# Kernel optimization log

Measured on AMD Instinct MI355X. Metric: run time of the kernel, lower is better.

## Reference

```python
import jax, jax.numpy as jnp
import numpy as np

B = 1024        # interactions per batch (graphs per side)
DIM = 64        # args.dim
HID = 64        # args.hidd_dim == args.word_dim
L = 2           # args.num_layers
NREL = 4        # relation types
N_USERS, N_ITEMS, N_WORDS = 100000, 50000, 50000
N = 131072      # total nodes per batched graph (per side)
E = 524288      # total edges per batched graph (per side)
D_FM = (L + 1) * DIM * 2  # 384


def setup_inputs() -> dict:
    key = jax.random.key(0)
    ks = iter(jax.random.split(key, 64))
    nrm = lambda shape, s=0.05: jax.random.normal(next(ks), shape, jnp.float32) * s
    ri = lambda shape, hi: jax.random.randint(next(ks), shape, 0, hi)
    # deterministic sorted graph-membership vector: equal-size graphs, no empty segments
    batch = (jnp.arange(N) * B) // N
    return dict(
        uid=ri((B,), N_USERS), iid=ri((B,), N_ITEMS),
        u_nodes=ri((N,), N_WORDS), i_nodes=ri((N,), N_WORDS),
        u_edge_index=ri((2, E), N), i_edge_index=ri((2, E), N),
        u_edge_type=ri((E,), NREL), i_edge_type=ri((E,), NREL),
        u_batch=batch, i_batch=batch,
        user_emb=nrm((N_USERS, DIM)), item_emb=nrm((N_ITEMS, DIM)), word_emb=nrm((N_WORDS, HID)),
        trans_u_W=nrm((L, DIM, HID)), trans_u_b=jnp.zeros((L, HID)),
        trans_i_W=nrm((L, DIM, HID)), trans_i_b=jnp.zeros((L, HID)),
        trans_w_W=nrm((L, HID, DIM)), trans_w_b=jnp.zeros((L, DIM)),
        inter_u_W=nrm((DIM, DIM)), inter_u_b=jnp.zeros((DIM,)),
        inter_i_W=nrm((DIM, DIM)), inter_i_b=jnp.zeros((DIM,)),
        conv_u_W=nrm((L, HID, HID)), conv_u_b=jnp.zeros((L, HID)),
        conv_u_att=nrm((L, 3, HID)), conv_u_rel=nrm((L, NREL, HID)),
        conv_i_W=nrm((L, HID, HID)), conv_i_b=jnp.zeros((L, HID)),
        conv_i_att=nrm((L, 3, HID)), conv_i_rel=nrm((L, NREL, HID)),
        pool_W=nrm((HID, HID)),
        fm_w=nrm((D_FM,)), fm_V=nrm((D_FM, D_FM)),
        fm_bias_u=jnp.zeros((N_USERS,)), fm_bias_i=jnp.zeros((N_ITEMS,)), fm_bias=jnp.zeros((1,)),
    )


def _gat(x, ei, et, W, b, att, rel):
    """Relational GAT conv: attention over incoming edges with relation-type term."""
    n = x.shape[0]
    h = x @ W + b                         # [n, HID]
    src, dst = ei[0], ei[1]
    e = jax.nn.leaky_relu(h[src] @ att[0] + h[dst] @ att[1] + rel[et] @ att[2], 0.2)  # [E]
    emax = jax.ops.segment_max(e, dst, num_segments=n)
    emax = jnp.where(jnp.isfinite(emax), emax, 0.0)   # guard nodes with no in-edges
    ex = jnp.exp(e - emax[dst])
    den = jax.ops.segment_sum(ex, dst, num_segments=n)
    alpha = ex / (den[dst] + 1e-16)
    return jax.nn.relu(jax.ops.segment_sum(alpha[:, None] * h[src], dst, num_segments=n))


def _conv_pool(ui_em, x, ei, et, batch, Ws, bs, atts, rels, tw_W, tw_b, pool_W, nb):
    """L stages of GAT conv -> query-conditioned soft pooling gate -> global max pool."""
    inv_sqrt_d = 1.0 / np.sqrt(HID).astype(np.float32)
    outs = []
    for i in range(L):
        x = _gat(x, ei, et, Ws[i], bs[i], atts[i], rels[i])
        q = ui_em[i]                                          # [B, HID] per-graph query
        score = jax.nn.sigmoid(jnp.sum((x @ pool_W) * q[batch], -1) * inv_sqrt_d)  # [N]
        x = x * score[:, None]
        pooled = jax.ops.segment_max(x, batch, num_segments=nb)  # gmp -> [B, HID]
        outs.append(jax.nn.relu(pooled @ tw_W[i] + tw_b[i]))     # trans_w -> [B, DIM]
    return jnp.concatenate(outs, -1)                             # [B, L*DIM]


def reference(uid, iid, u_nodes, i_nodes, u_edge_index, i_edge_index,
              u_edge_type, i_edge_type, u_batch, i_batch,
              user_emb, item_emb, word_emb,
              trans_u_W, trans_u_b, trans_i_W, trans_i_b, trans_w_W, trans_w_b,
              inter_u_W, inter_u_b, inter_i_W, inter_i_b,
              conv_u_W, conv_u_b, conv_u_att, conv_u_rel,
              conv_i_W, conv_i_b, conv_i_att, conv_i_rel,
              pool_W, fm_w, fm_V, fm_bias_u, fm_bias_i, fm_bias):
    u_e = user_emb[uid]                                        # [B, DIM]
    i_e = item_emb[iid]
    u_em = [jax.nn.relu(u_e @ trans_u_W[i] + trans_u_b[i]) for i in range(L)]
    i_em = [jax.nn.relu(i_e @ trans_i_W[i] + trans_i_b[i]) for i in range(L)]
    u_pool = _conv_pool(u_em, word_emb[u_nodes], u_edge_index, u_edge_type, u_batch,
                        conv_u_W, conv_u_b, conv_u_att, conv_u_rel,
                        trans_w_W, trans_w_b, pool_W, B)
    i_pool = _conv_pool(i_em, word_emb[i_nodes], i_edge_index, i_edge_type, i_batch,
                        conv_i_W, conv_i_b, conv_i_att, conv_i_rel,
                        trans_w_W, trans_w_b, pool_W, B)
    user_rep = jax.nn.relu(u_e @ inter_u_W + inter_u_b)
    item_rep = jax.nn.relu(i_e @ inter_i_W + inter_i_b)
    x = jnp.concatenate([user_rep, u_pool, item_rep, i_pool], -1)   # [B, D_FM]
    # FM layer (degree-2 interaction with full V matrix, as in source)
    linear = x @ fm_w                                               # [B]
    xv = x @ fm_V                                                   # [B, D_FM]
    mlp = 0.5 * jnp.sum(xv * xv - (x * x) @ (fm_V * fm_V), -1)
    return linear + mlp + fm_bias_u[uid] + fm_bias_i[iid] + fm_bias[0]
```

## Files before the change

kernel.cpp:

```cpp
#include <hip/hip_runtime.h>
#include <hip/hip_bf16.h>

#define NN 131072
#define NE 524288
#define NB 1024

typedef __attribute__((ext_vector_type(8))) short short8;
typedef __attribute__((ext_vector_type(4))) float f32x4;

__device__ __forceinline__ float wsum(float v){
#pragma unroll
  for (int o = 32; o > 0; o >>= 1) v += __shfl_xor(v, o, 64);
  return v;
}
__device__ __forceinline__ short f2bs(float f){
  __hip_bfloat16 t = __float2bfloat16(f);
  union { __hip_bfloat16 b; short s; } u; u.b = t; return u.s;
}
__device__ __forceinline__ float bs2f(short s){
  return __uint_as_float(((unsigned)(unsigned short)s) << 16);
}
__device__ __forceinline__ float ulo2f(unsigned v){ return __uint_as_float(v << 16); }
__device__ __forceinline__ float uhi2f(unsigned v){ return __uint_as_float(v & 0xFFFF0000u); }
__device__ __forceinline__ unsigned fpack(float x, float y){
  return (unsigned)(unsigned short)f2bs(x) | ((unsigned)(unsigned short)f2bs(y) << 16);
}

__global__ void k_mega(int wconvB,
                       const int* __restrict__ u_ei, const int* __restrict__ i_ei,
                       int* __restrict__ cnt, int* __restrict__ loff,
                       const float* __restrict__ wemb, unsigned* __restrict__ wtab,
                       int n32,
                       const float* __restrict__ cuW, const float* __restrict__ ciW,
                       const float* __restrict__ pW,
                       const float* __restrict__ cub, const float* __restrict__ cib,
                       const float* __restrict__ uatt, const float* __restrict__ iatt,
                       const float* __restrict__ urel, const float* __restrict__ irel,
                       short8* __restrict__ frag, float* __restrict__ waA,
                       float* __restrict__ ba, float* __restrict__ rtab,
                       const int* __restrict__ uid, const int* __restrict__ iid,
                       const float* __restrict__ uemb, const float* __restrict__ iemb,
                       const float* __restrict__ uiW, const float* __restrict__ uib,
                       const float* __restrict__ iiW, const float* __restrict__ iib,
                       const float* __restrict__ utW, const float* __restrict__ utb,
                       const float* __restrict__ itW, const float* __restrict__ itb,
                       float* __restrict__ xfm, float* __restrict__ q){
  const int histB = 2 * NE / 256;
  int blk = blockIdx.x, tid = threadIdx.x;
  if (blk < histB){
    int ee = blk * 256 + tid;
    int side = ee >= NE;
    int e = ee - side * NE;
    const int* ei = side ? i_ei : u_ei;
    int dst = ei[NE + e] + side * NN;
    int p = atomicAdd(&cnt[dst], 1);
    loff[ee] = p;
  } else if (blk < histB + 10){
    int b2 = blk - histB;
    int mat = b2 >> 1;
    const float* W = mat < 2 ? cuW + mat * 4096 : (mat < 4 ? ciW + (mat - 2) * 4096 : pW);
    int g = (b2 & 1) * 256 + tid;
    int lane = g & 63, rest = g >> 6;
    int hh = rest & 1, t = rest >> 1;
    int m = lane & 15, qq = lane >> 4;
    short8 v;
#pragma unroll
    for (int j = 0; j < 8; j++)
      v[j] = f2bs(W[(hh * 32 + qq * 8 + j) * 64 + (t * 16 + m)]);
    frag[mat * 512 + g] = v;
  } else if (blk < histB + 12){
    int side = blk - histB - 10;
    const float* W    = side ? ciW : cuW;
    const float* bias = side ? cib : cub;
    const float* att  = side ? iatt : uatt;
    const float* rel  = side ? irel : urel;
    int l = tid >> 7, a = (tid >> 6) & 1, kk = tid & 63;
    float s = 0.f;
    for (int c = 0; c < 64; c++) s += W[l * 4096 + kk * 64 + c] * att[l * 192 + a * 64 + c];
    waA[((side * 2 + l) * 2 + a) * 64 + kk] = s;
    if (tid < 4){
      int l2 = tid >> 1, a2 = tid & 1;
      float sb = 0.f;
      for (int c = 0; c < 64; c++) sb += bias[l2 * 64 + c] * att[l2 * 192 + a2 * 64 + c];
      ba[(side * 2 + l2) * 2 + a2] = sb;
    }
    if (tid >= 4 && tid < 12){
      int id = tid - 4, l2 = id >> 2, tt = id & 3;
      float sr = 0.f;
      for (int c = 0; c < 64; c++) sr += rel[l2 * 256 + tt * 64 + c] * att[l2 * 192 + 128 + c];
      rtab[(side * 2 + l2) * 4 + tt] = sr;
    }
  } else if (blk < histB + 12 + wconvB){
    int id = (blk - histB - 12) * 256 + tid;
    if (id < n32){
      const float2* src = (const float2*)wemb;
      float2 v = src[id];
      wtab[id] = fpack(v.x, v.y);
    }
  } else {
    int lane = tid & 63, w = tid >> 6;
    int b = (blk - histB - 12 - wconvB) * 4 + w;
    int side = b >= NB;
    int lb = b - side * NB;
    const int* ids = side ? iid : uid;
    const float* emb = side ? iemb : uemb;
    const float* interW = side ? iiW : uiW;
    const float* interB = side ? iib : uib;
    const float* transW = side ? itW : utW;
    const float* transB = side ? itb : utb;
    int repOff = side ? 192 : 0;
    float xe = emb[(long)ids[lb] * 64 + lane];
    float o = interB[lane];
#pragma unroll
    for (int k = 0; k < 64; k++) o += __shfl(xe, k, 64) * interW[k * 64 + lane];
    xfm[lb * 384 + repOff + lane] = fmaxf(o, 0.f);
    for (int l = 0; l < 2; l++){
      float t = transB[l * 64 + lane];
#pragma unroll
      for (int k = 0; k < 64; k++) t += __shfl(xe, k, 64) * transW[l * 4096 + k * 64 + lane];
      q[((size_t)(side * 2 + l) * NB + lb) * 64 + lane] = fmaxf(t, 0.f);
    }
  }
}

__global__ void k_scan1(const int* __restrict__ cnt, int* __restrict__ rowptr,
                        int* __restrict__ bsum){
  __shared__ int sh[256];
  int i = blockIdx.x * 256 + threadIdx.x;
  int v = cnt[i];
  sh[threadIdx.x] = v; __syncthreads();
  for (int off = 1; off < 256; off <<= 1){
    int t = (threadIdx.x >= off) ? sh[threadIdx.x - off] : 0;
    __syncthreads();
    sh[threadIdx.x] += t;
    __syncthreads();
  }
  int incl = sh[threadIdx.x];
  rowptr[i] = incl - v;
  if (threadIdx.x == 255) bsum[blockIdx.x] = incl;
}

__global__ void k_scan2(int* __restrict__ bsum){
  __shared__ int sh[1024];
  int v = bsum[threadIdx.x];
  sh[threadIdx.x] = v; __syncthreads();
  for (int off = 1; off < 1024; off <<= 1){
    int t = (threadIdx.x >= off) ? sh[threadIdx.x - off] : 0;
    __syncthreads();
    sh[threadIdx.x] += t;
    __syncthreads();
  }
  bsum[threadIdx.x] = sh[threadIdx.x] - v;
}

__global__ void k_scan3(int* __restrict__ rowptr, const int* __restrict__ bsum){
  int i = blockIdx.x * 256 + threadIdx.x;
  int v = rowptr[i] + bsum[blockIdx.x];
  rowptr[i] = v;
  if (i == 0) rowptr[2 * NN] = 2 * NE;
}

__global__ void k_scw(const int* __restrict__ u_ei, const int* __restrict__ i_ei,
                      const int* __restrict__ u_et, const int* __restrict__ i_et,
                      const int* __restrict__ rowptr, const int* __restrict__ loff,
                      int* __restrict__ pedge,
                      const short* __restrict__ wtab, int nwords,
                      const float* __restrict__ waA, const float* __restrict__ ba,
                      float* __restrict__ wa0, float* __restrict__ wa1){
  const int scatB = 2 * NE / 256;
  int blk = blockIdx.x, tid = threadIdx.x;
  if (blk < scatB){
    int ee = blk * 256 + tid;
    int side = ee >= NE;
    int e = ee - side * NE;
    const int* ei = side ? i_ei : u_ei;
    const int* et = side ? i_et : u_et;
    int dst = ei[NE + e] + side * NN;
    int src = ei[e] + side * NN;
    int p = rowptr[dst] + loff[ee];
    pedge[p] = src | (et[e] << 18);
  } else {
    int lane = tid & 63, w = tid >> 6;
    int q = lane >> 4, cl = lane & 15;
    int sw0 = ((blk - scatB) * 4 + w) * 8;
    const uint2* wt2 = (const uint2*)wtab;
    for (int it = 0; it < 2; it++){
      int wj = sw0 + it * 4 + q;
      if (wj >= 2 * nwords) continue;
      int side = wj >= nwords;
      int wid = wj - side * nwords;
      const float* A0 = waA + (side * 2 + 0) * 2 * 64;
      const float* A1 = A0 + 64;
      uint2 v = wt2[(long)wid * 16 + cl];
      int d = 4 * cl;
      float p0 = ulo2f(v.x) * A0[d] + uhi2f(v.x) * A0[d + 1] +
                 ulo2f(v.y) * A0[d + 2] + uhi2f(v.y) * A0[d + 3];
      float p1 = ulo2f(v.x) * A1[d] + uhi2f(v.x) * A1[d + 1] +
                 ulo2f(v.y) * A1[d + 2] + uhi2f(v.y) * A1[d + 3];
      p0 += __shfl_xor(p0, 1, 64); p0 += __shfl_xor(p0, 2, 64);
      p0 += __shfl_xor(p0, 4, 64); p0 += __shfl_xor(p0, 8, 64);
      p1 += __shfl_xor(p1, 1, 64); p1 += __shfl_xor(p1, 2, 64);
      p1 += __shfl_xor(p1, 4, 64); p1 += __shfl_xor(p1, 8, 64);
      if (cl == 0){
        wa0[(size_t)side * nwords + wid] = p0 + ba[side * 4 + 0];
        wa1[(size_t)side * nwords + wid] = p1 + ba[side * 4 + 1];
      }
    }
  }
}

template<int L>
__device__ __forceinline__ void dev_agg(
    const int* __restrict__ rowptr, const int* __restrict__ pedge,
    const float* __restrict__ a0, const float* __restrict__ a1,
    const float* __restrict__ wa0, const float* __restrict__ wa1,
    const int* __restrict__ u_nodes, const int* __restrict__ i_nodes, int nwords,
    const float* __restrict__ rtab, const short* __restrict__ rows,
    unsigned* __restrict__ xo32){
  int lane = threadIdx.x & 63, w = threadIdx.x >> 6;
  int nb = (blockIdx.x * 4 + w) * 8;
  int side = nb >= NN;
  const float* rt = rtab + (side * 2 + L) * 4;
  float rt0 = rt[0], rt1 = rt[1], rt2 = rt[2], rt3 = rt[3];
  const int* nodesS = side ? i_nodes : u_nodes;
  const float* wa0S = wa0 + (size_t)side * nwords;
  const float* wa1S = wa1 + (size_t)side * nwords;
  int q = lane >> 4, cl = lane & 15;
  int rp = (lane < 9) ? rowptr[nb + lane] : 0;
  float a1v = 0.f;
  if (L == 0){
    if (lane < 8) a1v = wa1S[nodesS[nb + lane - side * NN]];
  } else {
    if (lane < 8) a1v = a1[nb + lane];
  }
  int rp0 = __shfl(rp, 0, 64);
  int rp8 = __shfl(rp, 8, 64);
  int tot = min(rp8 - rp0, 64);
  int eidx = rp0 + lane;
  int pe = (lane < tot) ? pedge[eidx] : 0;
  int psrc = pe & 0x3FFFF;
  int prow; float pa0 = 0.f;
  if (L == 0){
    int wid = (lane < tot) ? nodesS[psrc - side * NN] : 0;
    prow = wid;
    if (lane < tot) pa0 = wa0S[wid];
  } else {
    prow = psrc;
    if (lane < tot) pa0 = a0[psrc];
  }
  int kn = 0;
#pragma unroll
  for (int t = 1; t < 8; t++)
    kn += (eidx >= __shfl(rp, t, 64)) ? 1 : 0;
  float a1n = __shfl(a1v, kn, 64);
  int pet = (pe >> 18) & 3;
  float rr = (pet & 2) ? ((pet & 1) ? rt3 : rt2) : ((pet & 1) ? rt1 : rt0);
  float vv = pa0 + a1n + rr;
  vv = (vv > 0.f) ? vv : 0.2f * vv;
  float pex = (lane < tot) ? __expf(vv) : 0.f;
  const uint2* h2 = (const uint2*)rows;
#pragma unroll
  for (int k = 0; k < 8; k++){
    int r0 = __shfl(rp, k, 64), r1 = __shfl(rp, k + 1, 64);
    float a1k = __shfl(a1v, k, 64);
    float ax0 = 0.f, ay0 = 0.f, ax1 = 0.f, ay1 = 0.f, den = 0.f;
    for (int j = r0; j < r1; j += 4){
      int e = j + q;
      bool ok = e < r1;
      int idx = e - rp0;
      int idxc = min(idx, 63);
      int s = __shfl(prow, idxc, 64);
      float ex = __shfl(pex, idxc, 64);
      if (idx >= 64 && ok){
        int pe2 = pedge[e];
        int s2 = pe2 & 0x3FFFF;
        int et2 = (pe2 >> 18) & 3;
        float r2 = (et2 & 2) ? ((et2 & 1) ? rt3 : rt2) : ((et2 & 1) ? rt1 : rt0);
        float av;
        if (L == 0){ int wid = nodesS[s2 - side * NN]; av = wa0S[wid]; s = wid; }
        else       { av = a0[s2]; s = s2; }
        float v2 = av + a1k + r2;
        v2 = (v2 > 0.f) ? v2 : 0.2f * v2;
        ex = __expf(v2);
      }
      if (ok){
        uint2 v = h2[(long)s * 16 + cl];
        ax0 += ex * ulo2f(v.x); ay0 += ex * uhi2f(v.x);
        ax1 += ex * ulo2f(v.y); ay1 += ex * uhi2f(v.y);
        den += ex;
      }
    }
    ax0 += __shfl_xor(ax0, 16, 64); ax0 += __shfl_xor(ax0, 32, 64);
    ay0 += __shfl_xor(ay0, 16, 64); ay0 += __shfl_xor(ay0, 32, 64);
    ax1 += __shfl_xor(ax1, 16, 64); ax1 += __shfl_xor(ax1, 32, 64);
    ay1 += __shfl_xor(ay1, 16, 64); ay1 += __shfl_xor(ay1, 32, 64);
    den += __shfl_xor(den, 16, 64); den += __shfl_xor(den, 32, 64);
    float inv = 1.f / (den + 1e-16f);
    if (q == 0){
      uint2 o;
      o.x = fpack(ax0 * inv, ay0 * inv);
      o.y = fpack(ax1 * inv, ay1 * inv);
      ((uint2*)xo32)[(long)(nb + k) * 16 + cl] = o;
    }
  }
}

__global__ __launch_bounds__(256) void k_agg0(
    const int* __restrict__ rowptr, const int* __restrict__ pedge,
    const float* __restrict__ wa0, const float* __restrict__ wa1,
    const int* __restrict__ u_nodes, const int* __restrict__ i_nodes, int nwords,
    const float* __restrict__ rtab, const short* __restrict__ wtab,
    unsigned* __restrict__ xo32){
  dev_agg<0>(rowptr, pedge, nullptr, nullptr, wa0, wa1, u_nodes, i_nodes, nwords,
             rtab, wtab, xo32);
}

__global__ __launch_bounds__(256) void k_agg1(
    const int* __restrict__ rowptr, const int* __restrict__ pedge,
    const float* __restrict__ a0, const float* __restrict__ a1,
    const float* __restrict__ rtab, const short* __restrict__ x,
    unsigned* __restrict__ xo32){
  dev_agg<1>(rowptr, pedge, a0, a1, nullptr, nullptr, nullptr, nullptr, 0,
             rtab, x, xo32);
}

__global__ __launch_bounds__(256) void k_gp(
    int l, const short* __restrict__ xagg, const short8* __restrict__ frag,
    const float* __restrict__ cub, const float* __restrict__ cib,
    const float* __restrict__ waA_all, const float* __restrict__ ba_all,
    const float* __restrict__ qbuf, const float* __restrict__ twW_all,
    const float* __restrict__ twb_all, float* __restrict__ xfm,
    short* __restrict__ xnext, float* __restrict__ a0, float* __restrict__ a1){
  __shared__ short xt[128 * 72];
  __shared__ float gates[128];
  __shared__ float red[4][64];
  int b = blockIdx.x;
  int side = b >= NB;
  int g = b - side * NB;
  long base = (long)side * NN + (long)g * 128;
  int tid = threadIdx.x, lane = tid & 63, w = tid >> 6;
  int m = lane & 15, q = lane >> 4;
  const short8* wfrag = frag + (side * 2 + l) * 512;
  const float* bias = (side ? cib : cub) + l * 64;
  short8 Bf[4][2];
#pragma unroll
  for (int t = 0; t < 4; t++)
#pragma unroll
    for (int hh = 0; hh < 2; hh++)
      Bf[t][hh] = wfrag[(t * 2 + hh) * 64 + lane];
  float bs[4];
#pragma unroll
  for (int t = 0; t < 4; t++) bs[t] = bias[t * 16 + m];
  f32x4 accA[2][4];
#pragma unroll
  for (int rb = 0; rb < 2; rb++){
    long n0 = base + w * 32 + rb * 16;
    const short8* xr = (const short8*)(xagg + (n0 + m) * 64);
    short8 A0 = xr[q];
    short8 A1 = xr[q + 4];
#pragma unroll
    for (int t = 0; t < 4; t++){
      f32x4 acc = (f32x4){bs[t], bs[t], bs[t], bs[t]};
      acc = __builtin_amdgcn_mfma_f32_16x16x32_bf16(A0, Bf[t][0], acc, 0, 0, 0);
      acc = __builtin_amdgcn_mfma_f32_16x16x32_bf16(A1, Bf[t][1], acc, 0, 0, 0);
#pragma unroll
      for (int r = 0; r < 4; r++) acc[r] = fmaxf(acc[r], 0.f);
      accA[rb][t] = acc;
#pragma unroll
      for (int r = 0; r < 4; r++)
        xt[(w * 32 + rb * 16 + q * 4 + r) * 72 + t * 16 + m] = f2bs(acc[r]);
    }
  }
  __syncthreads();
  const short8* pfrag = frag + 4 * 512;
  const float* qv_ = qbuf + ((size_t)(side * 2 + l) * NB + g) * 64;
  short8 Pf[4][2];
#pragma unroll
  for (int t = 0; t < 4; t++)
#pragma unroll
    for (int hh = 0; hh < 2; hh++)
      Pf[t][hh] = pfrag[(t * 2 + hh) * 64 + lane];
  float qv[4];
#pragma unroll
  for (int t = 0; t < 4; t++) qv[t] = qv_[t * 16 + m];
#pragma unroll
  for (int rb = 0; rb < 2; rb++){
    int rowb = w * 32 + rb * 16;
    short8 A0 = *(const short8*)(xt + (rowb + m) * 72 + q * 8);
    short8 A1 = *(const short8*)(xt + (rowb + m) * 72 + 32 + q * 8);
    f32x4 accp[4];
#pragma unroll
    for (int t = 0; t < 4; t++){
      accp[t] = (f32x4){0.f, 0.f, 0.f, 0.f};
      accp[t] = __builtin_amdgcn_mfma_f32_16x16x32_bf16(A0, Pf[t][0], accp[t], 0, 0, 0);
      accp[t] = __builtin_amdgcn_mfma_f32_16x16x32_bf16(A1, Pf[t][1], accp[t], 0, 0, 0);
    }
#pragma unroll
    for (int r = 0; r < 4; r++){
      float p = accp[0][r] * qv[0] + accp[1][r] * qv[1] +
                accp[2][r] * qv[2] + accp[3][r] * qv[3];
      p += __shfl_xor(p, 1, 64); p += __shfl_xor(p, 2, 64);
      p += __shfl_xor(p, 4, 64); p += __shfl_xor(p, 8, 64);
      if (m == 0)
        gates[rowb + q * 4 + r] = 1.f / (1.f + __expf(-p * 0.125f));
    }
  }
  __syncthreads();
  const unsigned* xt32 = (const unsigned*)xt;
  int c = lane & 31, half = lane >> 5;
  float mxx = 0.f, mxy = 0.f;
#pragma unroll
  for (int p = 0; p < 16; p++){
    int nn = w * 32 + 2 * p + half;
    unsigned v = xt32[nn * 36 + c];
    float gt = gates[nn];
    mxx = fmaxf(mxx, ulo2f(v) * gt);
    mxy = fmaxf(mxy, uhi2f(v) * gt);
  }
  mxx = fmaxf(mxx, __shfl_xor(mxx, 32, 64));
  mxy = fmaxf(mxy, __shfl_xor(mxy, 32, 64));
  if (half == 0){ red[w][2 * c] = mxx; red[w][2 * c + 1] = mxy; }
  __syncthreads();
  if (tid < 64){
    const float* twW = twW_all + l * 4096;
    const float* twb = twb_all + l * 64;
    int off = (side ? 256 : 64) + l * 64;
    float p = fmaxf(fmaxf(red[0][tid], red[1][tid]), fmaxf(red[2][tid], red[3][tid]));
    float o = twb[tid];
    red[0][tid] = p;
    __syncwarp();
    for (int d = 0; d < 64; d++) o += red[0][d] * twW[d * 64 + tid];
    xfm[g * 384 + off + tid] = fmaxf(o, 0.f);
  }
  if (l == 0){
#pragma unroll
    for (int p = 0; p < 4; p++){
      int row = p * 32 + (tid >> 3);
      int col8 = (tid & 7) * 8;
      float gt = gates[row];
      short8 v = *(const short8*)(xt + row * 72 + col8);
      short8 o;
#pragma unroll
      for (int j = 0; j < 8; j++) o[j] = f2bs(bs2f(v[j]) * gt);
      *(short8*)(xnext + (base + row) * 64 + col8) = o;
    }
    const float* wn0p = waA_all + ((side * 2 + 1) * 2 + 0) * 64;
    const float* wn1p = wn0p + 64;
    float wn0[4], wn1[4];
#pragma unroll
    for (int t = 0; t < 4; t++){ wn0[t] = wn0p[t * 16 + m]; wn1[t] = wn1p[t * 16 + m]; }
    float ban0 = ba_all[(side * 2 + 1) * 2 + 0];
    float ban1 = ba_all[(side * 2 + 1) * 2 + 1];
#pragma unroll
    for (int rb = 0; rb < 2; rb++)
#pragma unroll
      for (int r = 0; r < 4; r++){
        float p0 = accA[rb][0][r] * wn0[0] + accA[rb][1][r] * wn0[1] +
                   accA[rb][2][r] * wn0[2] + accA[rb][3][r] * wn0[3];
        float p1 = accA[rb][0][r] * wn1[0] + accA[rb][1][r] * wn1[1] +
                   accA[rb][2][r] * wn1[2] + accA[rb][3][r] * wn1[3];
        p0 += __shfl_xor(p0, 1, 64); p0 += __shfl_xor(p0, 2, 64);
        p0 += __shfl_xor(p0, 4, 64); p0 += __shfl_xor(p0, 8, 64);
        p1 += __shfl_xor(p1, 1, 64); p1 += __shfl_xor(p1, 2, 64);
        p1 += __shfl_xor(p1, 4, 64); p1 += __shfl_xor(p1, 8, 64);
        if (m == 0){
          int row = w * 32 + rb * 16 + q * 4 + r;
          float gr = gates[row];
          a0[base + row] = p0 * gr + ban0;
          a1[base + row] = p1 * gr + ban1;
        }
      }
  }
}

__global__ __launch_bounds__(384) void k_fm(
    const float* __restrict__ xfm, const float* __restrict__ V,
    const float* __restrict__ fw, const float* __restrict__ bu,
    const float* __restrict__ bi, const float* __restrict__ b0,
    const int* __restrict__ uid, const int* __restrict__ iid,
    float* __restrict__ out){
  __shared__ float xsh[4][384];
  __shared__ float xsq[4][384];
  __shared__ float part[4][384];
  int j = threadIdx.x;
  int g0 = blockIdx.x * 4;
#pragma unroll
  for (int b = 0; b < 4; b++){
    float xv_ = xfm[(g0 + b) * 384 + j];
    xsh[b][j] = xv_;
    xsq[b][j] = xv_ * xv_;
  }
  __syncthreads();
  float xv[4] = {0.f, 0.f, 0.f, 0.f};
  float vv[4] = {0.f, 0.f, 0.f, 0.f};
  for (int k = 0; k < 384; k++){
    float v = V[(size_t)k * 384 + j];
    float v2 = v * v;
#pragma unroll
    for (int b = 0; b < 4; b++){
      xv[b] = fmaf(xsh[b][k], v, xv[b]);
      vv[b] = fmaf(xsq[b][k], v2, vv[b]);
    }
  }
  float fwj = fw[j];
#pragma unroll
  for (int b = 0; b < 4; b++)
    part[b][j] = 0.5f * (xv[b] * xv[b] - vv[b]) + xsh[b][j] * fwj;
  __syncthreads();
  int w = j >> 6, lane = j & 63;
  if (w < 4){
    float s = part[w][lane] + part[w][lane + 64] + part[w][lane + 128] +
              part[w][lane + 192] + part[w][lane + 256] + part[w][lane + 320];
    s = wsum(s);
    if (lane == 0){
      int b = g0 + w;
      out[b] = s + bu[uid[b]] + bi[iid[b]] + b0[0];
    }
  }
}

extern "C" void kernel_launch(void* const* d_in, const int* in_sizes, int n_in,
                              void* d_out, int out_size, void* d_ws, size_t ws_size,
                              hipStream_t stream) {
  const int* uid      = (const int*)d_in[0];
  const int* iid      = (const int*)d_in[1];
  const int* u_nodes  = (const int*)d_in[2];
  const int* i_nodes  = (const int*)d_in[3];
  const int* u_ei     = (const int*)d_in[4];
  const int* i_ei     = (const int*)d_in[5];
  const int* u_et     = (const int*)d_in[6];
  const int* i_et     = (const int*)d_in[7];
  const float* user_emb = (const float*)d_in[10];
  const float* item_emb = (const float*)d_in[11];
  const float* word_emb = (const float*)d_in[12];
  const float* trans_u_W = (const float*)d_in[13];
  const float* trans_u_b = (const float*)d_in[14];
  const float* trans_i_W = (const float*)d_in[15];
  const float* trans_i_b = (const float*)d_in[16];
  const float* trans_w_W = (const float*)d_in[17];
  const float* trans_w_b = (const float*)d_in[18];
  const float* inter_u_W = (const float*)d_in[19];
  const float* inter_u_b = (const float*)d_in[20];
  const float* inter_i_W = (const float*)d_in[21];
  const float* inter_i_b = (const float*)d_in[22];
  const float* conv_u_W  = (const float*)d_in[23];
  const float* conv_u_b  = (const float*)d_in[24];
  const float* conv_u_att= (const float*)d_in[25];
  const float* conv_u_rel= (const float*)d_in[26];
  const float* conv_i_W  = (const float*)d_in[27];
  const float* conv_i_b  = (const float*)d_in[28];
  const float* conv_i_att= (const float*)d_in[29];
  const float* conv_i_rel= (const float*)d_in[30];
  const float* pool_W    = (const float*)d_in[31];
  const float* fm_w      = (const float*)d_in[32];
  const float* fm_V      = (const float*)d_in[33];
  const float* fm_bias_u = (const float*)d_in[34];
  const float* fm_bias_i = (const float*)d_in[35];
  const float* fm_bias   = (const float*)d_in[36];
  float* out = (float*)d_out;
  int n32 = in_sizes[12] / 2;
  int nwords = in_sizes[12] / 64;
  int wconvB = (n32 + 255) / 256;

  char* w = (char*)d_ws;
  short* X0   = (short*)w;          w += (size_t)2 * NN * 64 * 2;
  short* X1   = (short*)w;          w += (size_t)2 * NN * 64 * 2;
  short* wtab = (short*)w;          w += (size_t)in_sizes[12] * 2;
  int* pedge  = (int*)w;            w += (size_t)2 * NE * 4;
  int* loff   = (int*)w;            w += (size_t)2 * NE * 4;
  float* a0   = (float*)w;          w += (size_t)2 * NN * 4;
  float* a1   = (float*)w;          w += (size_t)2 * NN * 4;
  float* wa0  = (float*)w;          w += (size_t)2 * nwords * 4;
  float* wa1  = (float*)w;          w += (size_t)2 * nwords * 4;
  int* rowptr = (int*)w;            w += (size_t)(2 * NN + 256) * 4;
  int* cnt    = (int*)w;            w += (size_t)2 * NN * 4;
  int* bsum   = (int*)w;            w += 1024 * 4;
  short8* frag = (short8*)w;        w += (size_t)5 * 512 * 16;
  float* waA  = (float*)w;          w += 2 * 2 * 2 * 64 * 4;
  float* ba   = (float*)w;          w += 64;
  float* rtab = (float*)w;          w += 64;
  float* qbuf = (float*)w;          w += (size_t)4 * NB * 64 * 4;
  float* xfm  = (float*)w;          w += (size_t)NB * 384 * 4;

  hipMemsetAsync(cnt, 0, (size_t)2 * NN * 4, stream);

  int histB = 2 * NE / 256;
  int megaB = histB + 12 + wconvB + 2 * NB / 4;
  k_mega<<<megaB, 256, 0, stream>>>(wconvB, u_ei, i_ei, cnt, loff,
                                    word_emb, (unsigned*)wtab, n32,
                                    conv_u_W, conv_i_W, pool_W, conv_u_b, conv_i_b,
                                    conv_u_att, conv_i_att, conv_u_rel, conv_i_rel,
                                    frag, waA, ba, rtab,
                                    uid, iid, user_emb, item_emb,
                                    inter_u_W, inter_u_b, inter_i_W, inter_i_b,
                                    trans_u_W, trans_u_b, trans_i_W, trans_i_b,
                                    xfm, qbuf);
  k_scan1<<<2 * NN / 256, 256, 0, stream>>>(cnt, rowptr, bsum);
  k_scan2<<<1, 1024, 0, stream>>>(bsum);
  k_scan3<<<2 * NN / 256, 256, 0, stream>>>(rowptr, bsum);
  int wgB = (2 * nwords + 31) / 32;
  int scatB = 2 * NE / 256;
  k_scw<<<scatB + wgB, 256, 0, stream>>>(u_ei, i_ei, u_et, i_et, rowptr, loff,
                                         pedge, wtab, nwords, waA, ba, wa0, wa1);

  k_agg0<<<2 * NN / 32, 256, 0, stream>>>(rowptr, pedge, wa0, wa1,
                                          u_nodes, i_nodes, nwords, rtab,
                                          wtab, (unsigned*)X0);
  k_gp  <<<2 * NB, 256, 0, stream>>>(0, X0, frag, conv_u_b, conv_i_b, waA, ba,
                                     qbuf, trans_w_W, trans_w_b, xfm, X1, a0, a1);
  k_agg1<<<2 * NN / 32, 256, 0, stream>>>(rowptr, pedge, a0, a1, rtab,
                                          X1, (unsigned*)X0);
  k_gp  <<<2 * NB, 256, 0, stream>>>(1, X0, frag, conv_u_b, conv_i_b, waA, ba,
                                     qbuf, trans_w_W, trans_w_b, xfm,
                                     nullptr, nullptr, nullptr);

  k_fm<<<NB / 4, 384, 0, stream>>>(xfm, fm_V, fm_w, fm_bias_u, fm_bias_i, fm_bias,
                                   uid, iid, out);
}
```

Baseline: 429.9 us.

## Fuse edge aggregation into per-graph GEMM/pool kernel and pad histogram counters

The per-node attention aggregation is moved into the per-graph GEMM/pooling kernel. Each wave gathers and normalises its 32 nodes directly into the shared-memory tile, so the aggregated bf16 features no longer make a round trip through a global buffer. This also removes two kernel launches per forward pass. Separately, the degree-histogram counters are spaced 64 bytes apart to reduce atomic contention on shared cache lines, at the cost of a 16x larger memset and strided reads in the scan. The fused kernel runs the gather phase with fewer, longer-lived blocks, which may lower memory-level parallelism for the latency-bound gathers.

```diff
diff --git a/kernel.cpp b/kernel.cpp
--- a/kernel.cpp
+++ b/kernel.cpp
@@ -53,7 +53,7 @@
     int e = ee - side * NE;
     const int* ei = side ? i_ei : u_ei;
     int dst = ei[NE + e] + side * NN;
-    int p = atomicAdd(&cnt[dst], 1);
+    int p = atomicAdd(&cnt[dst << 4], 1);
     loff[ee] = p;
   } else if (blk < histB + 10){
     int b2 = blk - histB;
@@ -127,7 +127,7 @@
                         int* __restrict__ bsum){
   __shared__ int sh[256];
   int i = blockIdx.x * 256 + threadIdx.x;
-  int v = cnt[i];
+  int v = cnt[i << 4];
   sh[threadIdx.x] = v; __syncthreads();
   for (int off = 1; off < 256; off <<= 1){
     int t = (threadIdx.x >= off) ? sh[threadIdx.x - off] : 0;
@@ -210,138 +210,119 @@
 }
 
 template<int L>
-__device__ __forceinline__ void dev_agg(
+__global__ __launch_bounds__(256) void k_fused(
     const int* __restrict__ rowptr, const int* __restrict__ pedge,
-    const float* __restrict__ a0, const float* __restrict__ a1,
+    const float* __restrict__ a0in, const float* __restrict__ a1in,
     const float* __restrict__ wa0, const float* __restrict__ wa1,
     const int* __restrict__ u_nodes, const int* __restrict__ i_nodes, int nwords,
     const float* __restrict__ rtab, const short* __restrict__ rows,
-    unsigned* __restrict__ xo32){
-  int lane = threadIdx.x & 63, w = threadIdx.x >> 6;
-  int nb = (blockIdx.x * 4 + w) * 8;
-  int side = nb >= NN;
-  const float* rt = rtab + (side * 2 + L) * 4;
-  float rt0 = rt[0], rt1 = rt[1], rt2 = rt[2], rt3 = rt[3];
-  const int* nodesS = side ? i_nodes : u_nodes;
-  const float* wa0S = wa0 + (size_t)side * nwords;
-  const float* wa1S = wa1 + (size_t)side * nwords;
-  int q = lane >> 4, cl = lane & 15;
-  int rp = (lane < 9) ? rowptr[nb + lane] : 0;
-  float a1v = 0.f;
-  if (L == 0){
-    if (lane < 8) a1v = wa1S[nodesS[nb + lane - side * NN]];
-  } else {
-    if (lane < 8) a1v = a1[nb + lane];
-  }
-  int rp0 = __shfl(rp, 0, 64);
-  int rp8 = __shfl(rp, 8, 64);
-  int tot = min(rp8 - rp0, 64);
-  int eidx = rp0 + lane;
-  int pe = (lane < tot) ? pedge[eidx] : 0;
-  int psrc = pe & 0x3FFFF;
-  int prow; float pa0 = 0.f;
-  if (L == 0){
-    int wid = (lane < tot) ? nodesS[psrc - side * NN] : 0;
-    prow = wid;
-    if (lane < tot) pa0 = wa0S[wid];
-  } else {
-    prow = psrc;
-    if (lane < tot) pa0 = a0[psrc];
-  }
-  int kn = 0;
-#pragma unroll
-  for (int t = 1; t < 8; t++)
-    kn += (eidx >= __shfl(rp, t, 64)) ? 1 : 0;
-  float a1n = __shfl(a1v, kn, 64);
-  int pet = (pe >> 18) & 3;
-  float rr = (pet & 2) ? ((pet & 1) ? rt3 : rt2) : ((pet & 1) ? rt1 : rt0);
-  float vv = pa0 + a1n + rr;
-  vv = (vv > 0.f) ? vv : 0.2f * vv;
-  float pex = (lane < tot) ? __expf(vv) : 0.f;
-  const uint2* h2 = (const uint2*)rows;
-#pragma unroll
-  for (int k = 0; k < 8; k++){
-    int r0 = __shfl(rp, k, 64), r1 = __shfl(rp, k + 1, 64);
-    float a1k = __shfl(a1v, k, 64);
-    float ax0 = 0.f, ay0 = 0.f, ax1 = 0.f, ay1 = 0.f, den = 0.f;
-    for (int j = r0; j < r1; j += 4){
-      int e = j + q;
-      bool ok = e < r1;
-      int idx = e - rp0;
-      int idxc = min(idx, 63);
-      int s = __shfl(prow, idxc, 64);
-      float ex = __shfl(pex, idxc, 64);
-      if (idx >= 64 && ok){
-        int pe2 = pedge[e];
-        int s2 = pe2 & 0x3FFFF;
-        int et2 = (pe2 >> 18) & 3;
-        float r2 = (et2 & 2) ? ((et2 & 1) ? rt3 : rt2) : ((et2 & 1) ? rt1 : rt0);
-        float av;
-        if (L == 0){ int wid = nodesS[s2 - side * NN]; av = wa0S[wid]; s = wid; }
-        else       { av = a0[s2]; s = s2; }
-        float v2 = av + a1k + r2;
-        v2 = (v2 > 0.f) ? v2 : 0.2f * v2;
-        ex = __expf(v2);
-      }
-      if (ok){
-        uint2 v = h2[(long)s * 16 + cl];
-        ax0 += ex * ulo2f(v.x); ay0 += ex * uhi2f(v.x);
-        ax1 += ex * ulo2f(v.y); ay1 += ex * uhi2f(v.y);
-        den += ex;
-      }
-    }
-    ax0 += __shfl_xor(ax0, 16, 64); ax0 += __shfl_xor(ax0, 32, 64);
-    ay0 += __shfl_xor(ay0, 16, 64); ay0 += __shfl_xor(ay0, 32, 64);
-    ax1 += __shfl_xor(ax1, 16, 64); ax1 += __shfl_xor(ax1, 32, 64);
-    ay1 += __shfl_xor(ay1, 16, 64); ay1 += __shfl_xor(ay1, 32, 64);
-    den += __shfl_xor(den, 16, 64); den += __shfl_xor(den, 32, 64);
-    float inv = 1.f / (den + 1e-16f);
-    if (q == 0){
-      uint2 o;
-      o.x = fpack(ax0 * inv, ay0 * inv);
-      o.y = fpack(ax1 * inv, ay1 * inv);
-      ((uint2*)xo32)[(long)(nb + k) * 16 + cl] = o;
-    }
-  }
-}
-
-__global__ __launch_bounds__(256) void k_agg0(
-    const int* __restrict__ rowptr, const int* __restrict__ pedge,
-    const float* __restrict__ wa0, const float* __restrict__ wa1,
-    const int* __restrict__ u_nodes, const int* __restrict__ i_nodes, int nwords,
-    const float* __restrict__ rtab, const short* __restrict__ wtab,
-    unsigned* __restrict__ xo32){
-  dev_agg<0>(rowptr, pedge, nullptr, nullptr, wa0, wa1, u_nodes, i_nodes, nwords,
-             rtab, wtab, xo32);
-}
-
-__global__ __launch_bounds__(256) void k_agg1(
-    const int* __restrict__ rowptr, const int* __restrict__ pedge,
-    const float* __restrict__ a0, const float* __restrict__ a1,
-    const float* __restrict__ rtab, const short* __restrict__ x,
-    unsigned* __restrict__ xo32){
-  dev_agg<1>(rowptr, pedge, a0, a1, nullptr, nullptr, nullptr, nullptr, 0,
-             rtab, x, xo32);
-}
-
-__global__ __launch_bounds__(256) void k_gp(
-    int l, const short* __restrict__ xagg, const short8* __restrict__ frag,
+    const short8* __restrict__ frag,
     const float* __restrict__ cub, const float* __restrict__ cib,
     const float* __restrict__ waA_all, const float* __restrict__ ba_all,
     const float* __restrict__ qbuf, const float* __restrict__ twW_all,
     const float* __restrict__ twb_all, float* __restrict__ xfm,
-    short* __restrict__ xnext, float* __restrict__ a0, float* __restrict__ a1){
+    short* __restrict__ xnext, float* __restrict__ a0o, float* __restrict__ a1o){
   __shared__ short xt[128 * 72];
   __shared__ float gates[128];
   __shared__ float red[4][64];
   int b = blockIdx.x;
   int side = b >= NB;
   int g = b - side * NB;
-  long base = (long)side * NN + (long)g * 128;
+  int base = side * NN + g * 128;
   int tid = threadIdx.x, lane = tid & 63, w = tid >> 6;
-  int m = lane & 15, q = lane >> 4;
-  const short8* wfrag = frag + (side * 2 + l) * 512;
-  const float* bias = (side ? cib : cub) + l * 64;
+  int q = lane >> 4, m = lane & 15;
+
+  {
+    const float* rt = rtab + (side * 2 + L) * 4;
+    float rt0 = rt[0], rt1 = rt[1], rt2 = rt[2], rt3 = rt[3];
+    const int* nodesS = side ? i_nodes : u_nodes;
+    const float* wa0S = wa0 + (size_t)side * nwords;
+    const float* wa1S = wa1 + (size_t)side * nwords;
+    const uint2* h2 = (const uint2*)rows;
+    uint2* xin2 = (uint2*)xt;
+    for (int g2 = 0; g2 < 4; g2++){
+      int nb = base + w * 32 + g2 * 8;
+      int rp = (lane < 9) ? rowptr[nb + lane] : 0;
+      float a1v = 0.f;
+      if (L == 0){
+        if (lane < 8) a1v = wa1S[nodesS[nb + lane - side * NN]];
+      } else {
+        if (lane < 8) a1v = a1in[nb + lane];
+      }
+      int rp0 = __shfl(rp, 0, 64);
+      int rp8 = __shfl(rp, 8, 64);
+      int tot = min(rp8 - rp0, 64);
+      int eidx = rp0 + lane;
+      int pe = (lane < tot) ? pedge[eidx] : 0;
+      int psrc = pe & 0x3FFFF;
+      int prow; float pa0 = 0.f;
+      if (L == 0){
+        int wid = (lane < tot) ? nodesS[psrc - side * NN] : 0;
+        prow = wid;
+        if (lane < tot) pa0 = wa0S[wid];
+      } else {
+        prow = psrc;
+        if (lane < tot) pa0 = a0in[psrc];
+      }
+      int kn = 0;
+#pragma unroll
+      for (int t = 1; t < 8; t++)
+        kn += (eidx >= __shfl(rp, t, 64)) ? 1 : 0;
+      float a1n = __shfl(a1v, kn, 64);
+      int pet = (pe >> 18) & 3;
+      float rr = (pet & 2) ? ((pet & 1) ? rt3 : rt2) : ((pet & 1) ? rt1 : rt0);
+      float vv = pa0 + a1n + rr;
+      vv = (vv > 0.f) ? vv : 0.2f * vv;
+      float pex = (lane < tot) ? __expf(vv) : 0.f;
+#pragma unroll
+      for (int k = 0; k < 8; k++){
+        int r0 = __shfl(rp, k, 64), r1 = __shfl(rp, k + 1, 64);
+        float a1k = __shfl(a1v, k, 64);
+        float ax0 = 0.f, ay0 = 0.f, ax1 = 0.f, ay1 = 0.f, den = 0.f;
+        for (int j = r0; j < r1; j += 4){
+          int e = j + q;
+          bool ok = e < r1;
+          int idx = e - rp0;
+          int idxc = min(idx, 63);
+          int s = __shfl(prow, idxc, 64);
+          float ex = __shfl(pex, idxc, 64);
+          if (idx >= 64 && ok){
+            int pe2 = pedge[e];
+            int s2 = pe2 & 0x3FFFF;
+            int et2 = (pe2 >> 18) & 3;
+            float r2 = (et2 & 2) ? ((et2 & 1) ? rt3 : rt2) : ((et2 & 1) ? rt1 : rt0);
+            float av;
+            if (L == 0){ int wid = nodesS[s2 - side * NN]; av = wa0S[wid]; s = wid; }
+            else       { av = a0in[s2]; s = s2; }
+            float v2 = av + a1k + r2;
+            v2 = (v2 > 0.f) ? v2 : 0.2f * v2;
+            ex = __expf(v2);
+          }
+          if (ok){
+            uint2 v = h2[(long)s * 16 + m];
+            ax0 += ex * ulo2f(v.x); ay0 += ex * uhi2f(v.x);
+            ax1 += ex * ulo2f(v.y); ay1 += ex * uhi2f(v.y);
+            den += ex;
+          }
+        }
+        ax0 += __shfl_xor(ax0, 16, 64); ax0 += __shfl_xor(ax0, 32, 64);
+        ay0 += __shfl_xor(ay0, 16, 64); ay0 += __shfl_xor(ay0, 32, 64);
+        ax1 += __shfl_xor(ax1, 16, 64); ax1 += __shfl_xor(ax1, 32, 64);
+        ay1 += __shfl_xor(ay1, 16, 64); ay1 += __shfl_xor(ay1, 32, 64);
+        den += __shfl_xor(den, 16, 64); den += __shfl_xor(den, 32, 64);
+        float inv = 1.f / (den + 1e-16f);
+        if (q == 0){
+          uint2 o;
+          o.x = fpack(ax0 * inv, ay0 * inv);
+          o.y = fpack(ax1 * inv, ay1 * inv);
+          xin2[(w * 32 + g2 * 8 + k) * 18 + m] = o;
+        }
+      }
+    }
+  }
+
+  const short8* wfrag = frag + (side * 2 + L) * 512;
+  const float* bias = (side ? cib : cub) + L * 64;
   short8 Bf[4][2];
 #pragma unroll
   for (int t = 0; t < 4; t++)
@@ -354,10 +335,9 @@
   f32x4 accA[2][4];
 #pragma unroll
   for (int rb = 0; rb < 2; rb++){
-    long n0 = base + w * 32 + rb * 16;
-    const short8* xr = (const short8*)(xagg + (n0 + m) * 64);
-    short8 A0 = xr[q];
-    short8 A1 = xr[q + 4];
+    const short* xr = xt + (w * 32 + rb * 16 + m) * 72;
+    short8 A0 = *(const short8*)(xr + q * 8);
+    short8 A1 = *(const short8*)(xr + 32 + q * 8);
 #pragma unroll
     for (int t = 0; t < 4; t++){
       f32x4 acc = (f32x4){bs[t], bs[t], bs[t], bs[t]};
@@ -373,7 +353,7 @@
   }
   __syncthreads();
   const short8* pfrag = frag + 4 * 512;
-  const float* qv_ = qbuf + ((size_t)(side * 2 + l) * NB + g) * 64;
+  const float* qv_ = qbuf + ((size_t)(side * 2 + L) * NB + g) * 64;
   short8 Pf[4][2];
 #pragma unroll
   for (int t = 0; t < 4; t++)
@@ -422,9 +402,9 @@
   if (half == 0){ red[w][2 * c] = mxx; red[w][2 * c + 1] = mxy; }
   __syncthreads();
   if (tid < 64){
-    const float* twW = twW_all + l * 4096;
-    const float* twb = twb_all + l * 64;
-    int off = (side ? 256 : 64) + l * 64;
+    const float* twW = twW_all + L * 4096;
+    const float* twb = twb_all + L * 64;
+    int off = (side ? 256 : 64) + L * 64;
     float p = fmaxf(fmaxf(red[0][tid], red[1][tid]), fmaxf(red[2][tid], red[3][tid]));
     float o = twb[tid];
     red[0][tid] = p;
@@ -432,7 +412,7 @@
     for (int d = 0; d < 64; d++) o += red[0][d] * twW[d * 64 + tid];
     xfm[g * 384 + off + tid] = fmaxf(o, 0.f);
   }
-  if (l == 0){
+  if (L == 0){
 #pragma unroll
     for (int p = 0; p < 4; p++){
       int row = p * 32 + (tid >> 3);
@@ -442,7 +422,7 @@
       short8 o;
 #pragma unroll
       for (int j = 0; j < 8; j++) o[j] = f2bs(bs2f(v[j]) * gt);
-      *(short8*)(xnext + (base + row) * 64 + col8) = o;
+      *(short8*)(xnext + (long)(base + row) * 64 + col8) = o;
     }
     const float* wn0p = waA_all + ((side * 2 + 1) * 2 + 0) * 64;
     const float* wn1p = wn0p + 64;
@@ -466,8 +446,8 @@
         if (m == 0){
           int row = w * 32 + rb * 16 + q * 4 + r;
           float gr = gates[row];
-          a0[base + row] = p0 * gr + ban0;
-          a1[base + row] = p1 * gr + ban1;
+          a0o[base + row] = p0 * gr + ban0;
+          a1o[base + row] = p1 * gr + ban1;
         }
       }
   }
@@ -563,7 +543,6 @@
   int wconvB = (n32 + 255) / 256;
 
   char* w = (char*)d_ws;
-  short* X0   = (short*)w;          w += (size_t)2 * NN * 64 * 2;
   short* X1   = (short*)w;          w += (size_t)2 * NN * 64 * 2;
   short* wtab = (short*)w;          w += (size_t)in_sizes[12] * 2;
   int* pedge  = (int*)w;            w += (size_t)2 * NE * 4;
@@ -573,7 +552,7 @@
   float* wa0  = (float*)w;          w += (size_t)2 * nwords * 4;
   float* wa1  = (float*)w;          w += (size_t)2 * nwords * 4;
   int* rowptr = (int*)w;            w += (size_t)(2 * NN + 256) * 4;
-  int* cnt    = (int*)w;            w += (size_t)2 * NN * 4;
+  int* cnt    = (int*)w;            w += (size_t)2 * NN * 64;
   int* bsum   = (int*)w;            w += 1024 * 4;
   short8* frag = (short8*)w;        w += (size_t)5 * 512 * 16;
   float* waA  = (float*)w;          w += 2 * 2 * 2 * 64 * 4;
@@ -582,7 +561,7 @@
   float* qbuf = (float*)w;          w += (size_t)4 * NB * 64 * 4;
   float* xfm  = (float*)w;          w += (size_t)NB * 384 * 4;
 
-  hipMemsetAsync(cnt, 0, (size_t)2 * NN * 4, stream);
+  hipMemsetAsync(cnt, 0, (size_t)2 * NN * 64, stream);
 
   int histB = 2 * NE / 256;
   int megaB = histB + 12 + wconvB + 2 * NB / 4;
@@ -603,16 +582,16 @@
   k_scw<<<scatB + wgB, 256, 0, stream>>>(u_ei, i_ei, u_et, i_et, rowptr, loff,
                                          pedge, wtab, nwords, waA, ba, wa0, wa1);
 
-  k_agg0<<<2 * NN / 32, 256, 0, stream>>>(rowptr, pedge, wa0, wa1,
-                                          u_nodes, i_nodes, nwords, rtab,
-                                          wtab, (unsigned*)X0);
-  k_gp  <<<2 * NB, 256, 0, stream>>>(0, X0, frag, conv_u_b, conv_i_b, waA, ba,
-                                     qbuf, trans_w_W, trans_w_b, xfm, X1, a0, a1);
-  k_agg1<<<2 * NN / 32, 256, 0, stream>>>(rowptr, pedge, a0, a1, rtab,
-                                          X1, (unsigned*)X0);
-  k_gp  <<<2 * NB, 256, 0, stream>>>(1, X0, frag, conv_u_b, conv_i_b, waA, ba,
-                                     qbuf, trans_w_W, trans_w_b, xfm,
-                                     nullptr, nullptr, nullptr);
+  k_fused<0><<<2 * NB, 256, 0, stream>>>(rowptr, pedge, nullptr, nullptr,
+                                         wa0, wa1, u_nodes, i_nodes, nwords,
+                                         rtab, wtab, frag, conv_u_b, conv_i_b,
+                                         waA, ba, qbuf, trans_w_W, trans_w_b,
+                                         xfm, X1, a0, a1);
+  k_fused<1><<<2 * NB, 256, 0, stream>>>(rowptr, pedge, a0, a1,
+                                         nullptr, nullptr, nullptr, nullptr, 0,
+                                         rtab, X1, frag, conv_u_b, conv_i_b,
+                                         waA, ba, qbuf, trans_w_W, trans_w_b,
+                                         xfm, nullptr, nullptr, nullptr);
 
   k_fm<<<NB / 4, 384, 0, stream>>>(xfm, fm_V, fm_w, fm_bias_u, fm_bias_i, fm_bias,
                                    uid, iid, out);
```

New measurement: 496.1 us. 15.4% more time.
